# Optimization experiments

Measured on AMD Instinct MI355X. Metric: run time of the kernel, lower is better.

## Reference

```python
import jax, jax.numpy as jnp
import numpy as np

LATENT_DIM = 64
EDGE_DIM = 4
HIDDEN_DIM = 32
N_NODES = 100000
N_EDGES = 1600000


def setup_inputs() -> dict:
    key = jax.random.key(0)
    ks = jax.random.split(key, 10)
    x = jax.random.normal(ks[0], (N_NODES, LATENT_DIM), dtype=jnp.float32)
    edge_index = jax.random.randint(ks[1], (2, N_EDGES), 0, N_NODES, dtype=jnp.int64)
    d2 = 2 * LATENT_DIM
    def lin(k, fan_in, fan_out):
        bound = 1.0 / np.sqrt(fan_in)
        kw, kb = jax.random.split(k)
        W = jax.random.uniform(kw, (fan_in, fan_out), jnp.float32, -bound, bound)
        b = jax.random.uniform(kb, (fan_out,), jnp.float32, -bound, bound)
        return W, b
    W_direct, b_direct = lin(ks[2], d2, EDGE_DIM)
    W1, b1 = lin(ks[3], d2, HIDDEN_DIM)
    W2, b2 = lin(ks[4], HIDDEN_DIM, HIDDEN_DIM)
    W3, b3 = lin(ks[5], HIDDEN_DIM, EDGE_DIM)
    return {
        "x": x, "edge_index": edge_index,
        "W_direct": W_direct, "b_direct": b_direct,
        "W1": W1, "b1": b1, "W2": W2, "b2": b2, "W3": W3, "b3": b3,
    }


def reference(x, edge_index, W_direct, b_direct, W1, b1, W2, b2, W3, b3):
    src, tgt = edge_index[0], edge_index[1]
    xs = x[src]  # [E, L] gather
    xt = x[tgt]  # [E, L] gather
    # elementwise min/max then concat -> [E, 2L]
    x_cat = jnp.concatenate([jnp.minimum(xs, xt), jnp.maximum(xs, xt)], axis=-1)
    h = jax.nn.relu(x_cat @ W1 + b1)           # [E, H]; dropout = identity (eval)
    h = jax.nn.relu((h @ W2 + b2) + h)         # residual block
    edge_pred = h @ W3 + b3                    # [E, edge_dim]
    pred_direct = x_cat @ W_direct + b_direct  # direct linear path
    return edge_pred + pred_direct
```

## Files before the change

kernel.cpp:

```cpp
#include <hip/hip_runtime.h>

typedef __attribute__((ext_vector_type(8))) short short8;
typedef __attribute__((ext_vector_type(4))) float f32x4;
typedef __attribute__((ext_vector_type(4))) unsigned int u32x4;

constexpr int HID = 32;
constexpr int LAT = 64;
constexpr int EPB = 256;
constexpr int NFRAG  = 12;
constexpr int NFRAG2 = 2;
constexpr int NFRAG3 = 1;
constexpr int HW_STRIDE = 17;

__device__ __forceinline__ unsigned pk2(float lo, float hi) {
    unsigned r;
    asm("v_cvt_pk_bf16_f32 %0, %1, %2" : "=v"(r) : "v"(lo), "v"(hi));
    return r;
}
__device__ __forceinline__ void mnmx_word(unsigned a, unsigned b, unsigned& mn, unsigned& mx) {
    float al = __uint_as_float(a << 16), ah = __uint_as_float(a & 0xFFFF0000u);
    float bl = __uint_as_float(b << 16), bh = __uint_as_float(b & 0xFFFF0000u);
    mn = pk2(fminf(al, bl), fminf(ah, bh));
    mx = pk2(fmaxf(al, bl), fmaxf(ah, bh));
}
struct MnMx4 { unsigned w0, w1, x0, x1; };
__device__ __forceinline__ MnMx4 mnmx4(float4 a, float4 b) {
    MnMx4 r;
    r.w0 = pk2(fminf(a.x, b.x), fminf(a.y, b.y));
    r.w1 = pk2(fminf(a.z, b.z), fminf(a.w, b.w));
    r.x0 = pk2(fmaxf(a.x, b.x), fmaxf(a.y, b.y));
    r.x1 = pk2(fmaxf(a.z, b.z), fmaxf(a.w, b.w));
    return r;
}

__global__ __launch_bounds__(256) void cvt_x_kernel(const float* __restrict__ x,
                                                    unsigned short* __restrict__ xb, int n8) {
    int i = blockIdx.x * blockDim.x + threadIdx.x;
    if (i >= n8) return;
    const float4* p = (const float4*)x + (long)i * 2;
    float4 a = p[0], b = p[1];
    u32x4 v = { pk2(a.x, a.y), pk2(a.z, a.w), pk2(b.x, b.y), pk2(b.z, b.w) };
    ((u32x4*)xb)[i] = v;
}

__global__ __launch_bounds__(256) void build_frags_kernel(const float* __restrict__ W1,
                                                          const float* __restrict__ Wd,
                                                          const float* __restrict__ W2,
                                                          const float* __restrict__ W3,
                                                          unsigned short* __restrict__ fr,
                                                          unsigned short* __restrict__ fr2,
                                                          unsigned short* __restrict__ fr3) {
    int id = blockIdx.x * blockDim.x + threadIdx.x;
    if (id < NFRAG * 64) {
        int l = id & 63;
        int ft = id >> 6;
        int s = ft / 3, t = ft - s * 3;
        int g = l >> 4, c = l & 15;
        unsigned w[4];
        #pragma unroll
        for (int q = 0; q < 4; ++q) {
            int k = s * 32 + g * 8 + q * 2;
            float lo, hi;
            if (t < 2) { lo = W1[k * HID + t * 16 + c]; hi = W1[(k + 1) * HID + t * 16 + c]; }
            else { lo = (c < 4) ? Wd[k * 4 + c] : 0.0f; hi = (c < 4) ? Wd[(k + 1) * 4 + c] : 0.0f; }
            w[q] = pk2(lo, hi);
        }
        u32x4 v = { w[0], w[1], w[2], w[3] };
        ((u32x4*)fr)[ft * 64 + l] = v;
    } else if (id < (NFRAG + NFRAG2) * 64) {
        int f2 = id - NFRAG * 64;
        int l = f2 & 63;
        int t = f2 >> 6;
        int g = l >> 4, c = l & 15;
        int col = t * 16 + c;
        unsigned w[4];
        #pragma unroll
        for (int q = 0; q < 4; ++q) {
            int f0 = g * 4 + q;
            int f1 = f0 + 16;
            float lo = W2[f0 * HID + col] + (f0 == col ? 1.0f : 0.0f);
            float hi = W2[f1 * HID + col] + (f1 == col ? 1.0f : 0.0f);
            w[q] = pk2(lo, hi);
        }
        u32x4 v = { w[0], w[1], w[2], w[3] };
        ((u32x4*)fr2)[t * 64 + l] = v;
    } else if (id < (NFRAG + NFRAG2 + NFRAG3) * 64) {
        int l = id - (NFRAG + NFRAG2) * 64;
        int g = l >> 4, c = l & 15;
        unsigned w[4];
        #pragma unroll
        for (int q = 0; q < 4; ++q) {
            int f0 = g * 4 + q;
            int f1 = f0 + 16;
            float lo = (c < 4) ? W3[f0 * 4 + c] : 0.0f;
            float hi = (c < 4) ? W3[f1 * 4 + c] : 0.0f;
            w[q] = pk2(lo, hi);
        }
        u32x4 v = { w[0], w[1], w[2], w[3] };
        ((u32x4*)fr3)[l] = v;
    }
}

template<int XMODE>
__global__ __launch_bounds__(256, 4) void edge_mfma_kernel(
    const float* __restrict__ xf,
    const unsigned short* __restrict__ xb,
    const unsigned short* __restrict__ fr,
    const unsigned short* __restrict__ fr2,
    const unsigned short* __restrict__ fr3,
    const int* __restrict__ ei,
    const float* __restrict__ b1, const float* __restrict__ bd,
    const float* __restrict__ b2, const float* __restrict__ b3,
    float* __restrict__ out, int E)
{
    __shared__ unsigned hw[EPB][HW_STRIDE];
    __shared__ float4 ols[EPB];
    const int tid = threadIdx.x;
    const int l = tid & 63;
    const int wv = tid >> 6;
    const int g = l >> 4, r = l & 15;
    const long blockBase = (long)blockIdx.x * EPB;

    short8 bfr[NFRAG];
    #pragma unroll
    for (int f = 0; f < NFRAG; ++f) bfr[f] = ((const short8*)fr)[f * 64 + l];
    short8 w2f[NFRAG2];
    #pragma unroll
    for (int f = 0; f < NFRAG2; ++f) w2f[f] = ((const short8*)fr2)[f * 64 + l];
    short8 w3f = ((const short8*)fr3)[l];

    const float b1lo = b1[r], b1hi = b1[16 + r];
    const float b2lo = b2[r], b2hi = b2[16 + r];
    const float cinit = (r < 4) ? (bd[r] + b3[r]) : 0.0f;

    #pragma unroll
    for (int tile = 0; tile < 4; ++tile) {
        long e = blockBase + wv * 64 + tile * 16 + r;
        long ecl = (e < E) ? e : (long)(E - 1);
        int si = ei[ecl];
        int ti = ei[(long)E + ecl];

        union { short8 s; u32x4 u; } af0, af1, af2, af3;
        if (XMODE == 1) {
            const u32x4* ps = (const u32x4*)(xb + (long)si * LAT);
            const u32x4* pt = (const u32x4*)(xb + (long)ti * LAT);
            u32x4 sl = ps[g], sh = ps[4 + g];
            u32x4 tl = pt[g], th = pt[4 + g];
            #pragma unroll
            for (int q = 0; q < 4; ++q) {
                unsigned mn, mx;
                mnmx_word(sl[q], tl[q], mn, mx);
                af0.u[q] = mn; af2.u[q] = mx;
                mnmx_word(sh[q], th[q], mn, mx);
                af1.u[q] = mn; af3.u[q] = mx;
            }
        } else {
            const float4* ps = (const float4*)(xf + (long)si * LAT);
            const float4* pt = (const float4*)(xf + (long)ti * LAT);
            float4 sa = ps[2 * g], sb = ps[2 * g + 1], sc = ps[8 + 2 * g], sd = ps[9 + 2 * g];
            float4 ta = pt[2 * g], tb = pt[2 * g + 1], tc = pt[8 + 2 * g], td = pt[9 + 2 * g];
            MnMx4 m0 = mnmx4(sa, ta);
            MnMx4 m1 = mnmx4(sb, tb);
            MnMx4 m2 = mnmx4(sc, tc);
            MnMx4 m3 = mnmx4(sd, td);
            af0.u[0] = m0.w0; af0.u[1] = m0.w1; af2.u[0] = m0.x0; af2.u[1] = m0.x1;
            af0.u[2] = m1.w0; af0.u[3] = m1.w1; af2.u[2] = m1.x0; af2.u[3] = m1.x1;
            af1.u[0] = m2.w0; af1.u[1] = m2.w1; af3.u[0] = m2.x0; af3.u[1] = m2.x1;
            af1.u[2] = m3.w0; af1.u[3] = m3.w1; af3.u[2] = m3.x0; af3.u[3] = m3.x1;
        }

        f32x4 a0 = {0.f, 0.f, 0.f, 0.f}, a1 = a0;
        f32x4 a2 = {cinit, cinit, cinit, cinit};
        a0 = __builtin_amdgcn_mfma_f32_16x16x32_bf16(af0.s, bfr[0],  a0, 0, 0, 0);
        a1 = __builtin_amdgcn_mfma_f32_16x16x32_bf16(af0.s, bfr[1],  a1, 0, 0, 0);
        a2 = __builtin_amdgcn_mfma_f32_16x16x32_bf16(af0.s, bfr[2],  a2, 0, 0, 0);
        a0 = __builtin_amdgcn_mfma_f32_16x16x32_bf16(af1.s, bfr[3],  a0, 0, 0, 0);
        a1 = __builtin_amdgcn_mfma_f32_16x16x32_bf16(af1.s, bfr[4],  a1, 0, 0, 0);
        a2 = __builtin_amdgcn_mfma_f32_16x16x32_bf16(af1.s, bfr[5],  a2, 0, 0, 0);
        a0 = __builtin_amdgcn_mfma_f32_16x16x32_bf16(af2.s, bfr[6],  a0, 0, 0, 0);
        a1 = __builtin_amdgcn_mfma_f32_16x16x32_bf16(af2.s, bfr[7],  a1, 0, 0, 0);
        a2 = __builtin_amdgcn_mfma_f32_16x16x32_bf16(af2.s, bfr[8],  a2, 0, 0, 0);
        a0 = __builtin_amdgcn_mfma_f32_16x16x32_bf16(af3.s, bfr[9],  a0, 0, 0, 0);
        a1 = __builtin_amdgcn_mfma_f32_16x16x32_bf16(af3.s, bfr[10], a1, 0, 0, 0);
        a2 = __builtin_amdgcn_mfma_f32_16x16x32_bf16(af3.s, bfr[11], a2, 0, 0, 0);

        const int rowbase = wv * 64 + tile * 16 + g * 4;
        const int erow = wv * 64 + tile * 16 + r;

        #pragma unroll
        for (int p = 0; p < 4; ++p)
            hw[rowbase + p][r] = pk2(fmaxf(a0[p] + b1lo, 0.0f), fmaxf(a1[p] + b1hi, 0.0f));

        union { short8 s; u32x4 u; } hf;
        #pragma unroll
        for (int j = 0; j < 4; ++j) hf.u[j] = hw[erow][g * 4 + j];

        f32x4 d0 = {0.f, 0.f, 0.f, 0.f}, d1 = d0;
        d0 = __builtin_amdgcn_mfma_f32_16x16x32_bf16(hf.s, w2f[0], d0, 0, 0, 0);
        d1 = __builtin_amdgcn_mfma_f32_16x16x32_bf16(hf.s, w2f[1], d1, 0, 0, 0);

        #pragma unroll
        for (int p = 0; p < 4; ++p)
            hw[rowbase + p][r] = pk2(fmaxf(d0[p] + b2lo, 0.0f), fmaxf(d1[p] + b2hi, 0.0f));

        union { short8 s; u32x4 u; } hf2;
        #pragma unroll
        for (int j = 0; j < 4; ++j) hf2.u[j] = hw[erow][g * 4 + j];

        f32x4 d3 = __builtin_amdgcn_mfma_f32_16x16x32_bf16(hf2.s, w3f, a2, 0, 0, 0);

        if (r < 4) {
            #pragma unroll
            for (int p = 0; p < 4; ++p) ((float*)&ols[rowbase + p])[r] = d3[p];
        }
    }

    long e = blockBase + tid;
    if (e < E) ((float4*)out)[e] = ols[tid];
}

__global__ __launch_bounds__(256) void edge_pred_fp32_kernel(
    const float* __restrict__ x, const int* __restrict__ ei,
    const float* __restrict__ Wd, const float* __restrict__ bd,
    const float* __restrict__ W1, const float* __restrict__ b1,
    const float* __restrict__ W2, const float* __restrict__ b2,
    const float* __restrict__ W3, const float* __restrict__ b3,
    float* __restrict__ out, int E)
{
    int e = blockIdx.x * blockDim.x + threadIdx.x;
    if (e >= E) return;
    int s = ei[e];
    int t = ei[E + e];
    const float4* xs4 = (const float4*)(x + (long)s * 64);
    const float4* xt4 = (const float4*)(x + (long)t * 64);
    float h[HID];
    #pragma unroll
    for (int j = 0; j < HID; ++j) h[j] = b1[j];
    float d0 = bd[0], d1 = bd[1], d2 = bd[2], d3 = bd[3];
    #pragma unroll 2
    for (int c = 0; c < 16; ++c) {
        float4 a = xs4[c];
        float4 b = xt4[c];
        float mn[4] = {fminf(a.x,b.x), fminf(a.y,b.y), fminf(a.z,b.z), fminf(a.w,b.w)};
        float mx[4] = {fmaxf(a.x,b.x), fmaxf(a.y,b.y), fmaxf(a.z,b.z), fmaxf(a.w,b.w)};
        #pragma unroll
        for (int q = 0; q < 4; ++q) {
            int lidx = c * 4 + q;
            const float* wlo = W1 + lidx * HID;
            const float* whi = W1 + (64 + lidx) * HID;
            #pragma unroll
            for (int j = 0; j < HID; ++j) { h[j] += mn[q]*wlo[j]; h[j] += mx[q]*whi[j]; }
            const float* dlo = Wd + lidx * 4;
            const float* dhi = Wd + (64 + lidx) * 4;
            d0 += mn[q]*dlo[0] + mx[q]*dhi[0];
            d1 += mn[q]*dlo[1] + mx[q]*dhi[1];
            d2 += mn[q]*dlo[2] + mx[q]*dhi[2];
            d3 += mn[q]*dlo[3] + mx[q]*dhi[3];
        }
    }
    float h1[HID];
    #pragma unroll
    for (int j = 0; j < HID; ++j) h1[j] = fmaxf(h[j], 0.0f);
    float s2[HID];
    #pragma unroll
    for (int j = 0; j < HID; ++j) s2[j] = b2[j] + h1[j];
    #pragma unroll 4
    for (int k = 0; k < HID; ++k) {
        const float* w2r = W2 + k * HID;
        #pragma unroll
        for (int j = 0; j < HID; ++j) s2[j] += h1[k] * w2r[j];
    }
    float o0 = b3[0] + d0, o1 = b3[1] + d1, o2 = b3[2] + d2, o3 = b3[3] + d3;
    #pragma unroll
    for (int k = 0; k < HID; ++k) {
        float hk = fmaxf(s2[k], 0.0f);
        const float* w3r = W3 + k * 4;
        o0 += hk*w3r[0]; o1 += hk*w3r[1]; o2 += hk*w3r[2]; o3 += hk*w3r[3];
    }
    *(float4*)(out + (long)e * 4) = make_float4(o0, o1, o2, o3);
}

extern "C" void kernel_launch(void* const* d_in, const int* in_sizes, int n_in,
                              void* d_out, int out_size, void* d_ws, size_t ws_size,
                              hipStream_t stream) {
    const float* x  = (const float*)d_in[0];
    const int*   ei = (const int*)d_in[1];
    const float* Wd = (const float*)d_in[2];
    const float* bd = (const float*)d_in[3];
    const float* W1 = (const float*)d_in[4];
    const float* b1 = (const float*)d_in[5];
    const float* W2 = (const float*)d_in[6];
    const float* b2 = (const float*)d_in[7];
    const float* W3 = (const float*)d_in[8];
    const float* b3 = (const float*)d_in[9];
    float* out = (float*)d_out;

    int E  = in_sizes[1] / 2;
    int NN = in_sizes[0] / LAT;

    size_t fbytes  = (size_t)NFRAG  * 64 * 16;
    size_t f2bytes = (size_t)NFRAG2 * 64 * 16;
    size_t f3bytes = (size_t)NFRAG3 * 64 * 16;
    size_t fall    = fbytes + f2bytes + f3bytes;
    size_t fpad    = (fall + 255) & ~(size_t)255;
    size_t xbytes  = (size_t)NN * LAT * 2;

    int grid = (E + EPB - 1) / EPB;
    if (ws_size >= fpad + xbytes) {
        unsigned short* frg  = (unsigned short*)d_ws;
        unsigned short* frg2 = (unsigned short*)((char*)d_ws + fbytes);
        unsigned short* frg3 = (unsigned short*)((char*)d_ws + fbytes + f2bytes);
        unsigned short* xb   = (unsigned short*)((char*)d_ws + fpad);
        hipLaunchKernelGGL(build_frags_kernel, dim3(4), dim3(256), 0, stream,
                           W1, Wd, W2, W3, frg, frg2, frg3);
        int n8 = NN * LAT / 8;
        hipLaunchKernelGGL(cvt_x_kernel, dim3((n8 + 255) / 256), dim3(256), 0, stream, x, xb, n8);
        hipLaunchKernelGGL((edge_mfma_kernel<1>), dim3(grid), dim3(256), 0, stream,
                           x, xb, frg, frg2, frg3, ei, b1, bd, b2, b3, out, E);
    } else if (ws_size >= fall) {
        unsigned short* frg  = (unsigned short*)d_ws;
        unsigned short* frg2 = (unsigned short*)((char*)d_ws + fbytes);
        unsigned short* frg3 = (unsigned short*)((char*)d_ws + fbytes + f2bytes);
        hipLaunchKernelGGL(build_frags_kernel, dim3(4), dim3(256), 0, stream,
                           W1, Wd, W2, W3, frg, frg2, frg3);
        hipLaunchKernelGGL((edge_mfma_kernel<0>), dim3(grid), dim3(256), 0, stream,
                           x, (const unsigned short*)nullptr, frg, frg2, frg3,
                           ei, b1, bd, b2, b3, out, E);
    } else {
        hipLaunchKernelGGL(edge_pred_fp32_kernel, dim3((E + 255) / 256), dim3(256), 0, stream,
                           x, ei, Wd, bd, W1, b1, W2, b2, W3, b3, out, E);
    }
}
```

Baseline: 83.40 us.

## Keep MLP hidden state in registers via transposed MFMA and pipeline gathers

Swaps the MFMA operand order so each lane's output accumulators line up with the next layer's input fragment layout. This removes the LDS round trips for the hidden activations and the output staging buffer. Index loads are hoisted and node gathers are double-buffered across tiles to overlap memory with compute. It also fuses the weight-fragment and x-conversion prep kernels into a single launch and relaxes launch bounds to 2 blocks per CU, which lowers the occupancy target in exchange for more registers. Outputs become 16-byte stores from a quarter of the lanes instead of a coalesced block store.

```diff
diff --git a/kernel.cpp b/kernel.cpp
--- a/kernel.cpp
+++ b/kernel.cpp
@@ -10,7 +10,6 @@
 constexpr int NFRAG  = 12;
 constexpr int NFRAG2 = 2;
 constexpr int NFRAG3 = 1;
-constexpr int HW_STRIDE = 17;
 
 __device__ __forceinline__ unsigned pk2(float lo, float hi) {
     unsigned r;
@@ -33,76 +32,76 @@
     return r;
 }
 
-__global__ __launch_bounds__(256) void cvt_x_kernel(const float* __restrict__ x,
-                                                    unsigned short* __restrict__ xb, int n8) {
-    int i = blockIdx.x * blockDim.x + threadIdx.x;
-    if (i >= n8) return;
-    const float4* p = (const float4*)x + (long)i * 2;
-    float4 a = p[0], b = p[1];
-    u32x4 v = { pk2(a.x, a.y), pk2(a.z, a.w), pk2(b.x, b.y), pk2(b.z, b.w) };
-    ((u32x4*)xb)[i] = v;
-}
-
-__global__ __launch_bounds__(256) void build_frags_kernel(const float* __restrict__ W1,
-                                                          const float* __restrict__ Wd,
-                                                          const float* __restrict__ W2,
-                                                          const float* __restrict__ W3,
-                                                          unsigned short* __restrict__ fr,
-                                                          unsigned short* __restrict__ fr2,
-                                                          unsigned short* __restrict__ fr3) {
-    int id = blockIdx.x * blockDim.x + threadIdx.x;
-    if (id < NFRAG * 64) {
-        int l = id & 63;
-        int ft = id >> 6;
-        int s = ft / 3, t = ft - s * 3;
-        int g = l >> 4, c = l & 15;
-        unsigned w[4];
-        #pragma unroll
-        for (int q = 0; q < 4; ++q) {
-            int k = s * 32 + g * 8 + q * 2;
-            float lo, hi;
-            if (t < 2) { lo = W1[k * HID + t * 16 + c]; hi = W1[(k + 1) * HID + t * 16 + c]; }
-            else { lo = (c < 4) ? Wd[k * 4 + c] : 0.0f; hi = (c < 4) ? Wd[(k + 1) * 4 + c] : 0.0f; }
-            w[q] = pk2(lo, hi);
+__global__ __launch_bounds__(256) void prep_kernel(const float* __restrict__ x,
+                                                   const float* __restrict__ W1,
+                                                   const float* __restrict__ Wd,
+                                                   const float* __restrict__ W2,
+                                                   const float* __restrict__ W3,
+                                                   unsigned short* __restrict__ fr,
+                                                   unsigned short* __restrict__ fr2,
+                                                   unsigned short* __restrict__ fr3,
+                                                   unsigned short* __restrict__ xb, int n8) {
+    if (blockIdx.x < 4) {
+        int id = blockIdx.x * 256 + threadIdx.x;
+        if (id < NFRAG * 64) {
+            int l = id & 63;
+            int ft = id >> 6;
+            int s = ft / 3, t = ft - s * 3;
+            int g = l >> 4, c = l & 15;
+            unsigned w[4];
+            #pragma unroll
+            for (int q = 0; q < 4; ++q) {
+                int k = s * 32 + g * 8 + q * 2;
+                float lo, hi;
+                if (t < 2) { lo = W1[k * HID + t * 16 + c]; hi = W1[(k + 1) * HID + t * 16 + c]; }
+                else { lo = (c < 4) ? Wd[k * 4 + c] : 0.0f; hi = (c < 4) ? Wd[(k + 1) * 4 + c] : 0.0f; }
+                w[q] = pk2(lo, hi);
+            }
+            u32x4 v = { w[0], w[1], w[2], w[3] };
+            ((u32x4*)fr)[ft * 64 + l] = v;
+        } else if (id < (NFRAG + NFRAG2) * 64) {
+            int f2 = id - NFRAG * 64;
+            int l = f2 & 63;
+            int t = f2 >> 6;
+            int g = l >> 4, c = l & 15;
+            int col = t * 16 + c;
+            unsigned w[4];
+            #pragma unroll
+            for (int q = 0; q < 4; ++q) {
+                int kb = (q < 2) ? (g * 4 + 2 * q) : (16 + g * 4 + 2 * (q - 2));
+                float lo = W2[kb * HID + col] + (kb == col ? 1.0f : 0.0f);
+                float hi = W2[(kb + 1) * HID + col] + ((kb + 1) == col ? 1.0f : 0.0f);
+                w[q] = pk2(lo, hi);
+            }
+            u32x4 v = { w[0], w[1], w[2], w[3] };
+            ((u32x4*)fr2)[t * 64 + l] = v;
+        } else if (id < (NFRAG + NFRAG2 + NFRAG3) * 64) {
+            int l = id - (NFRAG + NFRAG2) * 64;
+            int g = l >> 4, c = l & 15;
+            unsigned w[4];
+            #pragma unroll
+            for (int q = 0; q < 4; ++q) {
+                int kb = (q < 2) ? (g * 4 + 2 * q) : (16 + g * 4 + 2 * (q - 2));
+                float lo = (c < 4) ? W3[kb * 4 + c] : 0.0f;
+                float hi = (c < 4) ? W3[(kb + 1) * 4 + c] : 0.0f;
+                w[q] = pk2(lo, hi);
+            }
+            u32x4 v = { w[0], w[1], w[2], w[3] };
+            ((u32x4*)fr3)[l] = v;
         }
-        u32x4 v = { w[0], w[1], w[2], w[3] };
-        ((u32x4*)fr)[ft * 64 + l] = v;
-    } else if (id < (NFRAG + NFRAG2) * 64) {
-        int f2 = id - NFRAG * 64;
-        int l = f2 & 63;
-        int t = f2 >> 6;
-        int g = l >> 4, c = l & 15;
-        int col = t * 16 + c;
-        unsigned w[4];
-        #pragma unroll
-        for (int q = 0; q < 4; ++q) {
-            int f0 = g * 4 + q;
-            int f1 = f0 + 16;
-            float lo = W2[f0 * HID + col] + (f0 == col ? 1.0f : 0.0f);
-            float hi = W2[f1 * HID + col] + (f1 == col ? 1.0f : 0.0f);
-            w[q] = pk2(lo, hi);
+    } else {
+        int i = (blockIdx.x - 4) * 256 + threadIdx.x;
+        if (i < n8) {
+            const float4* p = (const float4*)x + (long)i * 2;
+            float4 a = p[0], b = p[1];
+            u32x4 v = { pk2(a.x, a.y), pk2(a.z, a.w), pk2(b.x, b.y), pk2(b.z, b.w) };
+            ((u32x4*)xb)[i] = v;
         }
-        u32x4 v = { w[0], w[1], w[2], w[3] };
-        ((u32x4*)fr2)[t * 64 + l] = v;
-    } else if (id < (NFRAG + NFRAG2 + NFRAG3) * 64) {
-        int l = id - (NFRAG + NFRAG2) * 64;
-        int g = l >> 4, c = l & 15;
-        unsigned w[4];
-        #pragma unroll
-        for (int q = 0; q < 4; ++q) {
-            int f0 = g * 4 + q;
-            int f1 = f0 + 16;
-            float lo = (c < 4) ? W3[f0 * 4 + c] : 0.0f;
-            float hi = (c < 4) ? W3[f1 * 4 + c] : 0.0f;
-            w[q] = pk2(lo, hi);
-        }
-        u32x4 v = { w[0], w[1], w[2], w[3] };
-        ((u32x4*)fr3)[l] = v;
     }
 }
 
 template<int XMODE>
-__global__ __launch_bounds__(256, 4) void edge_mfma_kernel(
+__global__ __launch_bounds__(256, 2) void edge_mfma_kernel(
     const float* __restrict__ xf,
     const unsigned short* __restrict__ xb,
     const unsigned short* __restrict__ fr,
@@ -113,110 +112,119 @@
     const float* __restrict__ b2, const float* __restrict__ b3,
     float* __restrict__ out, int E)
 {
-    __shared__ unsigned hw[EPB][HW_STRIDE];
-    __shared__ float4 ols[EPB];
     const int tid = threadIdx.x;
     const int l = tid & 63;
     const int wv = tid >> 6;
     const int g = l >> 4, r = l & 15;
-    const long blockBase = (long)blockIdx.x * EPB;
+    const long waveBase = (long)blockIdx.x * EPB + wv * 64;
 
     short8 bfr[NFRAG];
     #pragma unroll
     for (int f = 0; f < NFRAG; ++f) bfr[f] = ((const short8*)fr)[f * 64 + l];
-    short8 w2f[NFRAG2];
-    #pragma unroll
-    for (int f = 0; f < NFRAG2; ++f) w2f[f] = ((const short8*)fr2)[f * 64 + l];
-    short8 w3f = ((const short8*)fr3)[l];
-
-    const float b1lo = b1[r], b1hi = b1[16 + r];
-    const float b2lo = b2[r], b2hi = b2[16 + r];
-    const float cinit = (r < 4) ? (bd[r] + b3[r]) : 0.0f;
-
-    #pragma unroll
-    for (int tile = 0; tile < 4; ++tile) {
-        long e = blockBase + wv * 64 + tile * 16 + r;
+    short8 w2t[NFRAG2];
+    #pragma unroll
+    for (int f = 0; f < NFRAG2; ++f) w2t[f] = ((const short8*)fr2)[f * 64 + l];
+    short8 w3t = ((const short8*)fr3)[l];
+
+    const float4 b1a = ((const float4*)b1)[g], b1b = ((const float4*)b1)[4 + g];
+    const float4 b2a = ((const float4*)b2)[g], b2b = ((const float4*)b2)[4 + g];
+    f32x4 a2init;
+    #pragma unroll
+    for (int p = 0; p < 4; ++p) a2init[p] = (g == 0) ? (bd[p] + b3[p]) : 0.0f;
+
+    int sidx[4], tidx[4];
+    #pragma unroll
+    for (int t = 0; t < 4; ++t) {
+        long e = waveBase + t * 16 + r;
         long ecl = (e < E) ? e : (long)(E - 1);
-        int si = ei[ecl];
-        int ti = ei[(long)E + ecl];
-
-        union { short8 s; u32x4 u; } af0, af1, af2, af3;
-        if (XMODE == 1) {
-            const u32x4* ps = (const u32x4*)(xb + (long)si * LAT);
-            const u32x4* pt = (const u32x4*)(xb + (long)ti * LAT);
-            u32x4 sl = ps[g], sh = ps[4 + g];
-            u32x4 tl = pt[g], th = pt[4 + g];
-            #pragma unroll
-            for (int q = 0; q < 4; ++q) {
-                unsigned mn, mx;
-                mnmx_word(sl[q], tl[q], mn, mx);
-                af0.u[q] = mn; af2.u[q] = mx;
-                mnmx_word(sh[q], th[q], mn, mx);
-                af1.u[q] = mn; af3.u[q] = mx;
-            }
-        } else {
-            const float4* ps = (const float4*)(xf + (long)si * LAT);
-            const float4* pt = (const float4*)(xf + (long)ti * LAT);
+        sidx[t] = ei[ecl];
+        tidx[t] = ei[(long)E + ecl];
+    }
+
+    auto compute_tile = [&](short8 af0, short8 af1, short8 af2, short8 af3, int t) {
+        f32x4 a0 = {0.f, 0.f, 0.f, 0.f}, a1 = a0;
+        f32x4 a2 = a2init;
+        a0 = __builtin_amdgcn_mfma_f32_16x16x32_bf16(bfr[0],  af0, a0, 0, 0, 0);
+        a1 = __builtin_amdgcn_mfma_f32_16x16x32_bf16(bfr[1],  af0, a1, 0, 0, 0);
+        a2 = __builtin_amdgcn_mfma_f32_16x16x32_bf16(bfr[2],  af0, a2, 0, 0, 0);
+        a0 = __builtin_amdgcn_mfma_f32_16x16x32_bf16(bfr[3],  af1, a0, 0, 0, 0);
+        a1 = __builtin_amdgcn_mfma_f32_16x16x32_bf16(bfr[4],  af1, a1, 0, 0, 0);
+        a2 = __builtin_amdgcn_mfma_f32_16x16x32_bf16(bfr[5],  af1, a2, 0, 0, 0);
+        a0 = __builtin_amdgcn_mfma_f32_16x16x32_bf16(bfr[6],  af2, a0, 0, 0, 0);
+        a1 = __builtin_amdgcn_mfma_f32_16x16x32_bf16(bfr[7],  af2, a1, 0, 0, 0);
+        a2 = __builtin_amdgcn_mfma_f32_16x16x32_bf16(bfr[8],  af2, a2, 0, 0, 0);
+        a0 = __builtin_amdgcn_mfma_f32_16x16x32_bf16(bfr[9],  af3, a0, 0, 0, 0);
+        a1 = __builtin_amdgcn_mfma_f32_16x16x32_bf16(bfr[10], af3, a1, 0, 0, 0);
+        a2 = __builtin_amdgcn_mfma_f32_16x16x32_bf16(bfr[11], af3, a2, 0, 0, 0);
+
+        union { short8 s; u32x4 u; } hf;
+        hf.u[0] = pk2(fmaxf(a0[0] + b1a.x, 0.0f), fmaxf(a0[1] + b1a.y, 0.0f));
+        hf.u[1] = pk2(fmaxf(a0[2] + b1a.z, 0.0f), fmaxf(a0[3] + b1a.w, 0.0f));
+        hf.u[2] = pk2(fmaxf(a1[0] + b1b.x, 0.0f), fmaxf(a1[1] + b1b.y, 0.0f));
+        hf.u[3] = pk2(fmaxf(a1[2] + b1b.z, 0.0f), fmaxf(a1[3] + b1b.w, 0.0f));
+
+        f32x4 d0 = {0.f, 0.f, 0.f, 0.f}, d1 = d0;
+        d0 = __builtin_amdgcn_mfma_f32_16x16x32_bf16(w2t[0], hf.s, d0, 0, 0, 0);
+        d1 = __builtin_amdgcn_mfma_f32_16x16x32_bf16(w2t[1], hf.s, d1, 0, 0, 0);
+
+        union { short8 s; u32x4 u; } hf2;
+        hf2.u[0] = pk2(fmaxf(d0[0] + b2a.x, 0.0f), fmaxf(d0[1] + b2a.y, 0.0f));
+        hf2.u[1] = pk2(fmaxf(d0[2] + b2a.z, 0.0f), fmaxf(d0[3] + b2a.w, 0.0f));
+        hf2.u[2] = pk2(fmaxf(d1[0] + b2b.x, 0.0f), fmaxf(d1[1] + b2b.y, 0.0f));
+        hf2.u[3] = pk2(fmaxf(d1[2] + b2b.z, 0.0f), fmaxf(d1[3] + b2b.w, 0.0f));
+
+        f32x4 d3 = __builtin_amdgcn_mfma_f32_16x16x32_bf16(w3t, hf2.s, a2, 0, 0, 0);
+
+        long e = waveBase + t * 16 + r;
+        if (g == 0 && e < E)
+            ((float4*)out)[e] = make_float4(d3[0], d3[1], d3[2], d3[3]);
+    };
+
+    if (XMODE == 1) {
+        u32x4 Asl, Ash, Atl, Ath, Bsl, Bsh, Btl, Bth;
+        #define GATHER(P, t) { \
+            const u32x4* ps = (const u32x4*)(xb + (long)sidx[t] * LAT); \
+            const u32x4* pt = (const u32x4*)(xb + (long)tidx[t] * LAT); \
+            P##sl = ps[g]; P##sh = ps[4 + g]; P##tl = pt[g]; P##th = pt[4 + g]; }
+        #define COMPUTE(P, t) { \
+            union { short8 s; u32x4 u; } af0, af1, af2, af3; \
+            _Pragma("unroll") \
+            for (int q = 0; q < 4; ++q) { \
+                unsigned mn, mx; \
+                mnmx_word(P##sl[q], P##tl[q], mn, mx); af0.u[q] = mn; af2.u[q] = mx; \
+                mnmx_word(P##sh[q], P##th[q], mn, mx); af1.u[q] = mn; af3.u[q] = mx; \
+            } \
+            compute_tile(af0.s, af1.s, af2.s, af3.s, t); }
+
+        GATHER(A, 0)
+        GATHER(B, 1)
+        COMPUTE(A, 0)
+        GATHER(A, 2)
+        COMPUTE(B, 1)
+        GATHER(B, 3)
+        COMPUTE(A, 2)
+        COMPUTE(B, 3)
+        #undef GATHER
+        #undef COMPUTE
+    } else {
+        #pragma unroll
+        for (int t = 0; t < 4; ++t) {
+            const float4* ps = (const float4*)(xf + (long)sidx[t] * LAT);
+            const float4* pt = (const float4*)(xf + (long)tidx[t] * LAT);
             float4 sa = ps[2 * g], sb = ps[2 * g + 1], sc = ps[8 + 2 * g], sd = ps[9 + 2 * g];
             float4 ta = pt[2 * g], tb = pt[2 * g + 1], tc = pt[8 + 2 * g], td = pt[9 + 2 * g];
             MnMx4 m0 = mnmx4(sa, ta);
             MnMx4 m1 = mnmx4(sb, tb);
             MnMx4 m2 = mnmx4(sc, tc);
             MnMx4 m3 = mnmx4(sd, td);
+            union { short8 s; u32x4 u; } af0, af1, af2, af3;
             af0.u[0] = m0.w0; af0.u[1] = m0.w1; af2.u[0] = m0.x0; af2.u[1] = m0.x1;
             af0.u[2] = m1.w0; af0.u[3] = m1.w1; af2.u[2] = m1.x0; af2.u[3] = m1.x1;
             af1.u[0] = m2.w0; af1.u[1] = m2.w1; af3.u[0] = m2.x0; af3.u[1] = m2.x1;
             af1.u[2] = m3.w0; af1.u[3] = m3.w1; af3.u[2] = m3.x0; af3.u[3] = m3.x1;
+            compute_tile(af0.s, af1.s, af2.s, af3.s, t);
         }
-
-        f32x4 a0 = {0.f, 0.f, 0.f, 0.f}, a1 = a0;
-        f32x4 a2 = {cinit, cinit, cinit, cinit};
-        a0 = __builtin_amdgcn_mfma_f32_16x16x32_bf16(af0.s, bfr[0],  a0, 0, 0, 0);
-        a1 = __builtin_amdgcn_mfma_f32_16x16x32_bf16(af0.s, bfr[1],  a1, 0, 0, 0);
-        a2 = __builtin_amdgcn_mfma_f32_16x16x32_bf16(af0.s, bfr[2],  a2, 0, 0, 0);
-        a0 = __builtin_amdgcn_mfma_f32_16x16x32_bf16(af1.s, bfr[3],  a0, 0, 0, 0);
-        a1 = __builtin_amdgcn_mfma_f32_16x16x32_bf16(af1.s, bfr[4],  a1, 0, 0, 0);
-        a2 = __builtin_amdgcn_mfma_f32_16x16x32_bf16(af1.s, bfr[5],  a2, 0, 0, 0);
-        a0 = __builtin_amdgcn_mfma_f32_16x16x32_bf16(af2.s, bfr[6],  a0, 0, 0, 0);
-        a1 = __builtin_amdgcn_mfma_f32_16x16x32_bf16(af2.s, bfr[7],  a1, 0, 0, 0);
-        a2 = __builtin_amdgcn_mfma_f32_16x16x32_bf16(af2.s, bfr[8],  a2, 0, 0, 0);
-        a0 = __builtin_amdgcn_mfma_f32_16x16x32_bf16(af3.s, bfr[9],  a0, 0, 0, 0);
-        a1 = __builtin_amdgcn_mfma_f32_16x16x32_bf16(af3.s, bfr[10], a1, 0, 0, 0);
-        a2 = __builtin_amdgcn_mfma_f32_16x16x32_bf16(af3.s, bfr[11], a2, 0, 0, 0);
-
-        const int rowbase = wv * 64 + tile * 16 + g * 4;
-        const int erow = wv * 64 + tile * 16 + r;
-
-        #pragma unroll
-        for (int p = 0; p < 4; ++p)
-            hw[rowbase + p][r] = pk2(fmaxf(a0[p] + b1lo, 0.0f), fmaxf(a1[p] + b1hi, 0.0f));
-
-        union { short8 s; u32x4 u; } hf;
-        #pragma unroll
-        for (int j = 0; j < 4; ++j) hf.u[j] = hw[erow][g * 4 + j];
-
-        f32x4 d0 = {0.f, 0.f, 0.f, 0.f}, d1 = d0;
-        d0 = __builtin_amdgcn_mfma_f32_16x16x32_bf16(hf.s, w2f[0], d0, 0, 0, 0);
-        d1 = __builtin_amdgcn_mfma_f32_16x16x32_bf16(hf.s, w2f[1], d1, 0, 0, 0);
-
-        #pragma unroll
-        for (int p = 0; p < 4; ++p)
-            hw[rowbase + p][r] = pk2(fmaxf(d0[p] + b2lo, 0.0f), fmaxf(d1[p] + b2hi, 0.0f));
-
-        union { short8 s; u32x4 u; } hf2;
-        #pragma unroll
-        for (int j = 0; j < 4; ++j) hf2.u[j] = hw[erow][g * 4 + j];
-
-        f32x4 d3 = __builtin_amdgcn_mfma_f32_16x16x32_bf16(hf2.s, w3f, a2, 0, 0, 0);
-
-        if (r < 4) {
-            #pragma unroll
-            for (int p = 0; p < 4; ++p) ((float*)&ols[rowbase + p])[r] = d3[p];
-        }
-    }
-
-    long e = blockBase + tid;
-    if (e < E) ((float4*)out)[e] = ols[tid];
+    }
 }
 
 __global__ __launch_bounds__(256) void edge_pred_fp32_kernel(
@@ -311,18 +319,19 @@
         unsigned short* frg2 = (unsigned short*)((char*)d_ws + fbytes);
         unsigned short* frg3 = (unsigned short*)((char*)d_ws + fbytes + f2bytes);
         unsigned short* xb   = (unsigned short*)((char*)d_ws + fpad);
-        hipLaunchKernelGGL(build_frags_kernel, dim3(4), dim3(256), 0, stream,
-                           W1, Wd, W2, W3, frg, frg2, frg3);
         int n8 = NN * LAT / 8;
-        hipLaunchKernelGGL(cvt_x_kernel, dim3((n8 + 255) / 256), dim3(256), 0, stream, x, xb, n8);
+        int prep_grid = 4 + (n8 + 255) / 256;
+        hipLaunchKernelGGL(prep_kernel, dim3(prep_grid), dim3(256), 0, stream,
+                           x, W1, Wd, W2, W3, frg, frg2, frg3, xb, n8);
         hipLaunchKernelGGL((edge_mfma_kernel<1>), dim3(grid), dim3(256), 0, stream,
                            x, xb, frg, frg2, frg3, ei, b1, bd, b2, b3, out, E);
     } else if (ws_size >= fall) {
         unsigned short* frg  = (unsigned short*)d_ws;
         unsigned short* frg2 = (unsigned short*)((char*)d_ws + fbytes);
         unsigned short* frg3 = (unsigned short*)((char*)d_ws + fbytes + f2bytes);
-        hipLaunchKernelGGL(build_frags_kernel, dim3(4), dim3(256), 0, stream,
-                           W1, Wd, W2, W3, frg, frg2, frg3);
+        hipLaunchKernelGGL(prep_kernel, dim3(4), dim3(256), 0, stream,
+                           x, W1, Wd, W2, W3, frg, frg2, frg3,
+                           (unsigned short*)nullptr, 0);
         hipLaunchKernelGGL((edge_mfma_kernel<0>), dim3(grid), dim3(256), 0, stream,
                            x, (const unsigned short*)nullptr, frg, frg2, frg3,
                            ei, b1, bd, b2, b3, out, E);
```

Result: faster. 77.74 us (-6.8%).
